# Optimization experiments

Hardware: AMD Instinct MI355X
Metric: run time of the kernel (lower is better)

## Reference

```python
import jax, jax.numpy as jnp
import numpy as np

D_MODEL = 2048
NUM_HEADS = 16
HEAD_DIM = D_MODEL // NUM_HEADS
SCALE = HEAD_DIM ** -0.5
ALPHA = 1.0


def setup_inputs() -> dict:
    key = jax.random.key(0)
    ks = jax.random.split(key, 9)
    B, T = 2, 2048
    s = 0.02
    w = lambda k: jax.random.normal(k, (D_MODEL, D_MODEL), jnp.float32) * s
    b = lambda k: jax.random.normal(k, (D_MODEL,), jnp.float32) * s
    return {
        'x': jax.random.normal(ks[0], (B, T, D_MODEL), jnp.float32),
        'q_w': w(ks[1]), 'q_b': b(ks[2]),
        'k_w': w(ks[3]), 'k_b': b(ks[4]),
        'v_w': w(ks[5]), 'v_b': b(ks[6]),
        'o_w': w(ks[7]), 'o_b': b(ks[8]),
    }


def reference(x, q_w, q_b, k_w, k_b, v_w, v_b, o_w, o_b):
    B, T, D = x.shape
    H, HD = NUM_HEADS, HEAD_DIM

    def proj_split(w, bias):
        y = x @ w.T + bias  # torch Linear: x @ W^T + b
        # B T (H D) -> (B H) T D
        return y.reshape(B, T, H, HD).transpose(0, 2, 1, 3).reshape(B * H, T, HD)

    Q = proj_split(q_w, q_b)
    K = proj_split(k_w, k_b)
    V = proj_split(v_w, v_b)

    # Note: original computes S[h,i,j] = K_i . Q_j (K first, Q second)
    S = jnp.einsum('hid,hjd->hij', K, Q) * SCALE  # (B*H, T, T)

    idx = jnp.arange(T)
    delta = idx[:, None] - idx[None, :]  # delta[i,j] = i - j
    # similarity_power_law decay: -(delta**alpha) for delta>=0, else 0
    decay = jnp.where(delta < 0, 0.0, -(delta.astype(jnp.float32) ** ALPHA))
    # causal mask: positions with j > i (delta < 0) set to -inf, then add decay
    S = jnp.where(delta < 0, -jnp.inf, S) + decay

    C = jax.nn.softmax(S, axis=-1)
    attn = jnp.einsum('hij,hjd->hid', C, V)  # (B*H, T, HD)
    # (B H) T D -> B T (H D)
    attn = attn.reshape(B, H, T, HD).transpose(0, 2, 1, 3).reshape(B, T, D)
    return attn @ o_w.T + o_b
```

## Files before the change

kernel.cpp:

```cpp
#include <hip/hip_runtime.h>
#include <hip/hip_bf16.h>
#include <stdint.h>

#define BT    4096
#define DM    2048
#define TSEQ  2048
#define NHEAD 16
#define HD    128
#define QKV_LD 6144
#define ATT_SCALE 0.088388347648318447f
#define WIN   64

typedef __attribute__((ext_vector_type(8))) short short8;
typedef __attribute__((ext_vector_type(4))) float f32x4;

__device__ __forceinline__ uint16_t f2bf(float f) {
  uint32_t u = __float_as_uint(f);
  return (uint16_t)((u + 0x7FFFu + ((u >> 16) & 1u)) >> 16);
}

__device__ __forceinline__ void gload_lds16(const void* g, void* l) {
  __builtin_amdgcn_global_load_lds((__attribute__((address_space(1))) void*)g,
                                   (__attribute__((address_space(3))) void*)l,
                                   16, 0, 0);
}

__global__ __launch_bounds__(256) void prep(const float* __restrict__ x,
                                            const float* __restrict__ qw,
                                            const float* __restrict__ kw,
                                            const float* __restrict__ vw,
                                            const float* __restrict__ ow,
                                            const float* __restrict__ qb,
                                            const float* __restrict__ kb,
                                            const float* __restrict__ vb,
                                            uint16_t* __restrict__ xb,
                                            uint16_t* __restrict__ wqkv,
                                            uint16_t* __restrict__ wo,
                                            float* __restrict__ bcat) {
  const int NX = BT * DM / 4;
  const int NW = DM * DM / 4;
  const int total = NX + 4 * NW;
  int i0 = blockIdx.x * 256 + threadIdx.x;
  for (int idx = i0; idx < total; idx += gridDim.x * 256) {
    const float* src;
    uint16_t* dst;
    int off;
    if (idx < NX)            { src = x;  dst = xb;                          off = idx; }
    else if (idx < NX + NW)  { src = qw; dst = wqkv;                        off = idx - NX; }
    else if (idx < NX + 2*NW){ src = kw; dst = wqkv + (size_t)DM * DM;      off = idx - NX - NW; }
    else if (idx < NX + 3*NW){ src = vw; dst = wqkv + (size_t)2 * DM * DM;  off = idx - NX - 2*NW; }
    else                     { src = ow; dst = wo;                          off = idx - NX - 3*NW; }
    float4 v = ((const float4*)src)[off];
    ushort4 o;
    o.x = f2bf(v.x); o.y = f2bf(v.y); o.z = f2bf(v.z); o.w = f2bf(v.w);
    ((ushort4*)dst)[off] = o;
  }
  if (i0 < 3 * DM) {
    float v = (i0 < DM) ? qb[i0] : (i0 < 2 * DM ? kb[i0 - DM] : vb[i0 - 2 * DM]);
    bcat[i0] = v;
  }
}

__global__ __launch_bounds__(512, 1) void gemm384(const uint16_t* __restrict__ A,
                                                  const uint16_t* __restrict__ B,
                                                  const float* __restrict__ bias,
                                                  uint16_t* __restrict__ Cout) {
  __shared__ uint16_t sm[81920];

  const int tid = threadIdx.x;
  const int l   = tid & 63;
  const int wid = tid >> 6;
  const int wr  = wid >> 2;
  const int wc  = wid & 3;
  const int ln  = l & 15;
  const int g   = l >> 4;

  const int bid = blockIdx.x;
  const int xcd = bid & 7;
  const int idx = bid >> 3;
  const int m0  = ((xcd >> 2) * 8 + (idx >> 2)) << 8;
  const int n0  = ((xcd & 3) * 4 + (idx & 3)) * 384;

  const int s_r = wid * 8 + (l >> 3);
  const int s_c = ((l & 7) ^ ((wid * 4 + (l >> 4)) & 7)) << 3;
  const uint16_t* gA = A + (size_t)(m0 + s_r) * DM + s_c;
  const uint16_t* gB = B + (size_t)(n0 + s_r) * DM + s_c;
  const int sdst = wid * 512;

  const int key  = (ln >> 1) & 7;
  const int pc0  = (g ^ key) << 3;
  const int pc1  = ((4 + g) ^ key) << 3;
  const int aoff = (wr * 128 + ln) * 64;
  const int boff = 16384 + (wc * 96 + ln) * 64;

  f32x4 acc[8][6];
#pragma unroll
  for (int i = 0; i < 8; ++i)
#pragma unroll
    for (int j = 0; j < 6; ++j) acc[i][j] = (f32x4){0.f, 0.f, 0.f, 0.f};

  const int nt = DM >> 6;

#define STA(T, U)                                                                \
  if ((T) < nt) {                                                                \
    const uint16_t* s_ = gA + (size_t)((U) * 128) * DM + (size_t)(T) * 64;       \
    uint16_t* d_ = sm + ((T) & 1) * 40960 + (U) * 8192 + sdst;                   \
    gload_lds16(s_, d_);                                                         \
    gload_lds16(s_ + (size_t)64 * DM, d_ + 4096);                                \
  }
#define STB(T, U)                                                                \
  if ((T) < nt) {                                                                \
    const uint16_t* s_ = gB + (size_t)((U) * 128) * DM + (size_t)(T) * 64;       \
    uint16_t* d_ = sm + ((T) & 1) * 40960 + 16384 + (U) * 8192 + sdst;           \
    gload_lds16(s_, d_);                                                         \
    gload_lds16(s_ + (size_t)64 * DM, d_ + 4096);                                \
  }
#define FENCE() asm volatile("" ::: "memory")

#define MMH(BUFP, MH, PC)                                                        \
  __builtin_amdgcn_s_setprio(1);                                                 \
  _Pragma("unroll")                                                              \
  for (int mi = 0; mi < 4; ++mi) {                                               \
    short8 af = *(const short8*)((BUFP) + aoff + ((MH) * 64 + mi * 16) * 64 + (PC)); \
    _Pragma("unroll")                                                            \
    for (int nj = 0; nj < 6; ++nj)                                               \
      acc[(MH) * 4 + mi][nj] = __builtin_amdgcn_mfma_f32_16x16x32_bf16(          \
          af, bf[nj], acc[(MH) * 4 + mi][nj], 0, 0, 0);                          \
  }                                                                              \
  __builtin_amdgcn_s_setprio(0);

  STA(0, 0); STA(0, 1);
  STB(0, 0); STB(0, 1); STB(0, 2);
  STB(1, 0); STB(1, 1); STB(1, 2);
  asm volatile("s_waitcnt vmcnt(6)" ::: "memory");
  FENCE(); __builtin_amdgcn_s_barrier(); FENCE();

#pragma unroll 1
  for (int t = 0; t < nt; ++t) {
    const uint16_t* bufp = sm + (size_t)(t & 1) * 40960;
    short8 bf[6];
#pragma unroll
    for (int nj = 0; nj < 6; ++nj)
      bf[nj] = *(const short8*)(bufp + boff + nj * 1024 + pc0);
    STA(t + 1, 0);
    MMH(bufp, 0, pc0);
    STA(t + 1, 1);
    MMH(bufp, 1, pc0);
#pragma unroll
    for (int nj = 0; nj < 6; ++nj)
      bf[nj] = *(const short8*)(bufp + boff + nj * 1024 + pc1);
    MMH(bufp, 0, pc1);
    FENCE(); __builtin_amdgcn_s_barrier(); FENCE();
    STB(t + 2, 0); STB(t + 2, 1); STB(t + 2, 2);
    MMH(bufp, 1, pc1);
    FENCE();
    if (t < nt - 2)       asm volatile("s_waitcnt vmcnt(6)" ::: "memory");
    else if (t == nt - 2) asm volatile("s_waitcnt vmcnt(0)" ::: "memory");
    __builtin_amdgcn_s_barrier(); FENCE();
  }
#undef MMH
#undef STA
#undef STB

  const int g4 = g * 4;
#pragma unroll
  for (int a = 0; a < 8; ++a) {
    size_t row = (size_t)(m0 + wr * 128 + (a >> 2) * 64 + (a & 3) * 16 + g4);
#pragma unroll
    for (int nj = 0; nj < 6; ++nj) {
      int col = n0 + wc * 96 + nj * 16 + ln;
      float bv = bias[col];
#pragma unroll
      for (int r = 0; r < 4; ++r)
        Cout[(row + r) * QKV_LD + col] = f2bf(acc[a][nj][r] + bv);
    }
  }
}

__global__ __launch_bounds__(512, 1) void gemmO(const uint16_t* __restrict__ A,
                                                const uint16_t* __restrict__ B,
                                                const float* __restrict__ bias,
                                                float* __restrict__ Cout) {
  __shared__ uint16_t sm[49152];

  const int tid = threadIdx.x;
  const int l   = tid & 63;
  const int wid = tid >> 6;
  const int wr  = wid >> 2;
  const int wc  = wid & 3;
  const int ln  = l & 15;
  const int g   = l >> 4;

  const int bid = blockIdx.x;
  const int xcd = bid & 7;
  const int idx = bid >> 3;
  const int m0  = ((xcd >> 2) * 8 + (idx >> 2)) << 8;
  const int n0  = ((xcd & 3) * 4 + (idx & 3)) << 7;

  const int s_r = wid * 8 + (l >> 3);
  const int s_c = ((l & 7) ^ ((wid * 4 + (l >> 4)) & 7)) << 3;
  const uint16_t* gA = A + (size_t)(m0 + s_r) * DM + s_c;
  const uint16_t* gB = B + (size_t)(n0 + s_r) * DM + s_c;
  const int sdst = wid * 512;

  const int key  = (ln >> 1) & 7;
  const int pc0  = (g ^ key) << 3;
  const int pc1  = ((4 + g) ^ key) << 3;
  const int aoff = (wr * 128 + ln) * 64;
  const int boff = 16384 + (wc * 32 + ln) * 64;

  f32x4 acc[8][2];
#pragma unroll
  for (int i = 0; i < 8; ++i)
#pragma unroll
    for (int j = 0; j < 2; ++j) acc[i][j] = (f32x4){0.f, 0.f, 0.f, 0.f};

  const int nt = DM >> 6;

#define STA(T, U)                                                                \
  if ((T) < nt) {                                                                \
    const uint16_t* s_ = gA + (size_t)((U) * 128) * DM + (size_t)(T) * 64;       \
    uint16_t* d_ = sm + ((T) & 1) * 24576 + (U) * 8192 + sdst;                   \
    gload_lds16(s_, d_);                                                         \
    gload_lds16(s_ + (size_t)64 * DM, d_ + 4096);                                \
  }
#define STB(T)                                                                   \
  if ((T) < nt) {                                                                \
    const uint16_t* s_ = gB + (size_t)(T) * 64;                                  \
    uint16_t* d_ = sm + ((T) & 1) * 24576 + 16384 + sdst;                        \
    gload_lds16(s_, d_);                                                         \
    gload_lds16(s_ + (size_t)64 * DM, d_ + 4096);                                \
  }
#define FENCE() asm volatile("" ::: "memory")

#define MMH(BUFP, MH, PC)                                                        \
  __builtin_amdgcn_s_setprio(1);                                                 \
  _Pragma("unroll")                                                              \
  for (int mi = 0; mi < 4; ++mi) {                                               \
    short8 af = *(const short8*)((BUFP) + aoff + ((MH) * 64 + mi * 16) * 64 + (PC)); \
    _Pragma("unroll")                                                            \
    for (int nj = 0; nj < 2; ++nj)                                               \
      acc[(MH) * 4 + mi][nj] = __builtin_amdgcn_mfma_f32_16x16x32_bf16(          \
          af, bf[nj], acc[(MH) * 4 + mi][nj], 0, 0, 0);                          \
  }                                                                              \
  __builtin_amdgcn_s_setprio(0);

  STA(0, 0); STA(0, 1);
  STB(0);
  STB(1);
  asm volatile("s_waitcnt vmcnt(2)" ::: "memory");
  FENCE(); __builtin_amdgcn_s_barrier(); FENCE();

#pragma unroll 1
  for (int t = 0; t < nt; ++t) {
    const uint16_t* bufp = sm + (size_t)(t & 1) * 24576;
    short8 bf[2];
#pragma unroll
    for (int nj = 0; nj < 2; ++nj)
      bf[nj] = *(const short8*)(bufp + boff + nj * 1024 + pc0);
    STA(t + 1, 0);
    MMH(bufp, 0, pc0);
    STA(t + 1, 1);
    MMH(bufp, 1, pc0);
#pragma unroll
    for (int nj = 0; nj < 2; ++nj)
      bf[nj] = *(const short8*)(bufp + boff + nj * 1024 + pc1);
    MMH(bufp, 0, pc1);
    FENCE(); __builtin_amdgcn_s_barrier(); FENCE();
    STB(t + 2);
    MMH(bufp, 1, pc1);
    FENCE();
    if (t < nt - 2)       asm volatile("s_waitcnt vmcnt(2)" ::: "memory");
    else if (t == nt - 2) asm volatile("s_waitcnt vmcnt(0)" ::: "memory");
    __builtin_amdgcn_s_barrier(); FENCE();
  }
#undef MMH
#undef STA
#undef STB
#undef FENCE

  const int g4 = g * 4;
#pragma unroll
  for (int a = 0; a < 8; ++a) {
    size_t row = (size_t)(m0 + wr * 128 + (a >> 2) * 64 + (a & 3) * 16 + g4);
#pragma unroll
    for (int nj = 0; nj < 2; ++nj) {
      int col = n0 + wc * 32 + nj * 16 + ln;
      float bv = bias[col];
#pragma unroll
      for (int r = 0; r < 4; ++r)
        Cout[(row + r) * DM + col] = acc[a][nj][r] + bv;
    }
  }
}

__global__ __launch_bounds__(256) void attn_mfma(const uint16_t* __restrict__ QKV,
                                                 uint16_t* __restrict__ O) {
  __shared__ __align__(16) uint16_t smem[16384 + 17408];
  uint16_t* Qs = smem;
  uint16_t* Vt = smem + 16384;
  uint16_t* Pl = smem;

  const int tid  = threadIdx.x;
  const int lane = tid & 63;
  const int w    = tid >> 6;
  const int g    = lane >> 4;
  const int ln   = lane & 15;

  const int i0 = blockIdx.x * 64;
  const int h  = blockIdx.y;
  const int b  = blockIdx.z;
  const int wb = i0 - 63;
  const size_t hoff  = (size_t)h * HD;
  const size_t bbase = (size_t)b * TSEQ;

#pragma unroll
  for (int it = 0; it < 8; ++it) {
    int s   = it * 256 + tid;
    int row = s >> 4, c = s & 15;
    int j = wb + row;
    if (j >= 0 && j < TSEQ) {
      const uint16_t* gsrc = QKV + (bbase + j) * (size_t)QKV_LD + hoff
                           + (size_t)((c ^ (row & 7)) * 8);
      uint16_t* ldst = Qs + (size_t)(s & ~63) * 8;
      gload_lds16(gsrc, ldst);
    } else {
      uint4 z = {0, 0, 0, 0};
      *(uint4*)(Qs + (size_t)s * 8) = z;
    }
  }

#pragma unroll
  for (int it = 0; it < 4; ++it) {
    int s  = it * 256 + tid;
    int jp = (s & 15) | (it << 4);
    int dc = (s >> 4) & 15;
    int j0 = wb + 2 * jp;
    uint4 va = {0, 0, 0, 0}, vb = {0, 0, 0, 0};
    if (j0 >= 0 && j0 < TSEQ)
      va = *(const uint4*)(QKV + (bbase + j0) * (size_t)QKV_LD + 2 * DM + hoff + dc * 8);
    if (j0 + 1 >= 0 && j0 + 1 < TSEQ)
      vb = *(const uint4*)(QKV + (bbase + j0 + 1) * (size_t)QKV_LD + 2 * DM + hoff + dc * 8);
    const uint16_t* ap = (const uint16_t*)&va;
    const uint16_t* bp = (const uint16_t*)&vb;
#pragma unroll
    for (int t = 0; t < 8; ++t) {
      uint32_t pk = (uint32_t)ap[t] | ((uint32_t)bp[t] << 16);
      *(uint32_t*)(Vt + (size_t)(dc * 8 + t) * 136 + 2 * jp) = pk;
    }
  }

  short8 kreg[4];
  {
    const uint16_t* kp = QKV + (bbase + i0 + w * 16 + ln) * (size_t)QKV_LD
                       + DM + hoff + g * 8;
#pragma unroll
    for (int kc = 0; kc < 4; ++kc) kreg[kc] = *(const short8*)(kp + kc * 32);
  }

  __syncthreads();

  f32x4 acc[8];
#pragma unroll
  for (int nf = 0; nf < 8; ++nf) acc[nf] = (f32x4){0.f, 0.f, 0.f, 0.f};
#pragma unroll
  for (int kc = 0; kc < 4; ++kc) {
#pragma unroll
    for (int nf = 0; nf < 8; ++nf) {
      int row = nf * 16 + ln;
      int chunk = (kc * 4 + g) ^ (row & 7);
      short8 qf = *(const short8*)(Qs + (size_t)row * 128 + chunk * 8);
      acc[nf] = __builtin_amdgcn_mfma_f32_16x16x32_bf16(kreg[kc], qf, acc[nf], 0, 0, 0);
    }
  }

#pragma unroll
  for (int nf = 0; nf < 8; ++nf) {
    int rj = nf * 16 + ln;
    int jg = wb + rj;
#pragma unroll
    for (int r = 0; r < 4; ++r) {
      int il = w * 16 + g * 4 + r;
      int delta = il + 63 - rj;
      float v = acc[nf][r] * ATT_SCALE - (float)delta;
      acc[nf][r] = ((unsigned)delta < 64u && jg >= 0) ? v : -1e30f;
    }
  }

  float inv[4];
#pragma unroll
  for (int r = 0; r < 4; ++r) {
    float mx = acc[0][r];
#pragma unroll
    for (int nf = 1; nf < 8; ++nf) mx = fmaxf(mx, acc[nf][r]);
    mx = fmaxf(mx, __shfl_xor(mx, 1));
    mx = fmaxf(mx, __shfl_xor(mx, 2));
    mx = fmaxf(mx, __shfl_xor(mx, 4));
    mx = fmaxf(mx, __shfl_xor(mx, 8));
    float s = 0.f;
#pragma unroll
    for (int nf = 0; nf < 8; ++nf) {
      float e = __expf(acc[nf][r] - mx);
      acc[nf][r] = e;
      s += e;
    }
    s += __shfl_xor(s, 1);
    s += __shfl_xor(s, 2);
    s += __shfl_xor(s, 4);
    s += __shfl_xor(s, 8);
    inv[r] = 1.0f / s;
  }

  __syncthreads();

#pragma unroll
  for (int nf = 0; nf < 8; ++nf)
#pragma unroll
    for (int r = 0; r < 4; ++r)
      Pl[(size_t)(w * 16 + g * 4 + r) * 136 + nf * 16 + ln] = f2bf(acc[nf][r]);
  asm volatile("s_waitcnt lgkmcnt(0)" ::: "memory");
  __builtin_amdgcn_sched_barrier(0);

  f32x4 o[8];
#pragma unroll
  for (int nf = 0; nf < 8; ++nf) o[nf] = (f32x4){0.f, 0.f, 0.f, 0.f};
#pragma unroll
  for (int kc = 0; kc < 4; ++kc) {
    short8 pa = *(const short8*)(Pl + (size_t)(w * 16 + ln) * 136 + kc * 32 + g * 8);
#pragma unroll
    for (int nf = 0; nf < 8; ++nf) {
      short8 vbf = *(const short8*)(Vt + (size_t)(nf * 16 + ln) * 136 + kc * 32 + g * 8);
      o[nf] = __builtin_amdgcn_mfma_f32_16x16x32_bf16(pa, vbf, o[nf], 0, 0, 0);
    }
  }

  const size_t obase = (bbase + i0 + w * 16) * (size_t)DM + hoff;
#pragma unroll
  for (int nf = 0; nf < 8; ++nf)
#pragma unroll
    for (int r = 0; r < 4; ++r)
      O[obase + (size_t)(g * 4 + r) * DM + nf * 16 + ln] = f2bf(o[nf][r] * inv[r]);
}

extern "C" void kernel_launch(void* const* d_in, const int* in_sizes, int n_in,
                              void* d_out, int out_size, void* d_ws, size_t ws_size,
                              hipStream_t stream) {
  const float* x   = (const float*)d_in[0];
  const float* q_w = (const float*)d_in[1];
  const float* q_b = (const float*)d_in[2];
  const float* k_w = (const float*)d_in[3];
  const float* k_b = (const float*)d_in[4];
  const float* v_w = (const float*)d_in[5];
  const float* v_b = (const float*)d_in[6];
  const float* o_w = (const float*)d_in[7];
  const float* o_b = (const float*)d_in[8];

  char* ws = (char*)d_ws;
  const size_t XB_BYTES   = (size_t)BT * DM * 2;
  const size_t W_BYTES    = (size_t)DM * DM * 2;
  const size_t WQKV_BYTES = 3 * W_BYTES;

  uint16_t* xb   = (uint16_t*)(ws);
  uint16_t* wqkv = (uint16_t*)(ws + XB_BYTES);
  uint16_t* wo   = (uint16_t*)(ws + XB_BYTES + WQKV_BYTES);
  float*    bcat = (float*)   (ws + XB_BYTES + WQKV_BYTES + W_BYTES);
  uint16_t* QKVb = (uint16_t*)(ws + XB_BYTES + WQKV_BYTES + W_BYTES + 24576);

  prep<<<2048, 256, 0, stream>>>(x, q_w, k_w, v_w, o_w, q_b, k_b, v_b,
                                 xb, wqkv, wo, bcat);

  gemm384<<<256, 512, 0, stream>>>(xb, wqkv, bcat, QKVb);

  dim3 ga(TSEQ / 64, NHEAD, 2);
  attn_mfma<<<ga, 256, 0, stream>>>(QKVb, xb);

  gemmO<<<256, 512, 0, stream>>>(xb, wo, o_b, (float*)d_out);
}
```

Measured before the change: 172.3 us.

## Load A operand of output GEMM directly into registers, stage only B in LDS

The output projection GEMM now reads its A fragments straight from global memory into registers, prefetching the next k-tile into a second register set, instead of staging A through LDS. LDS is used only for B, shrinking shared memory from 96KB to 32KB and removing A's LDS reads. The aim is to cut LDS traffic and bandwidth pressure in the main loop. In exchange it raises register pressure (32 short8 fragments held live) and relies on direct, less coalesced global loads. Each A row is also read redundantly by the four column waves that share it.

```diff
diff --git a/kernel.cpp b/kernel.cpp
--- a/kernel.cpp
+++ b/kernel.cpp
@@ -177,11 +177,11 @@
   }
 }
 
-__global__ __launch_bounds__(512, 1) void gemmO(const uint16_t* __restrict__ A,
-                                                const uint16_t* __restrict__ B,
-                                                const float* __restrict__ bias,
-                                                float* __restrict__ Cout) {
-  __shared__ uint16_t sm[49152];
+__global__ __launch_bounds__(512, 1) void gemmO3(const uint16_t* __restrict__ A,
+                                                 const uint16_t* __restrict__ B,
+                                                 const float* __restrict__ bias,
+                                                 float* __restrict__ Cout) {
+  __shared__ uint16_t sm[16384];
 
   const int tid = threadIdx.x;
   const int l   = tid & 63;
@@ -197,17 +197,17 @@
   const int m0  = ((xcd >> 2) * 8 + (idx >> 2)) << 8;
   const int n0  = ((xcd & 3) * 4 + (idx & 3)) << 7;
 
+  const uint16_t* gAf = A + (size_t)(m0 + wr * 128 + ln) * DM + (g << 3);
+
   const int s_r = wid * 8 + (l >> 3);
   const int s_c = ((l & 7) ^ ((wid * 4 + (l >> 4)) & 7)) << 3;
-  const uint16_t* gA = A + (size_t)(m0 + s_r) * DM + s_c;
   const uint16_t* gB = B + (size_t)(n0 + s_r) * DM + s_c;
   const int sdst = wid * 512;
 
   const int key  = (ln >> 1) & 7;
   const int pc0  = (g ^ key) << 3;
   const int pc1  = ((4 + g) ^ key) << 3;
-  const int aoff = (wr * 128 + ln) * 64;
-  const int boff = 16384 + (wc * 32 + ln) * 64;
+  const int boff = (wc * 32 + ln) * 64;
 
   f32x4 acc[8][2];
 #pragma unroll
@@ -217,79 +217,88 @@
 
   const int nt = DM >> 6;
 
-#define STA(T, U)                                                                \
+#define STB3(T)                                                                  \
   if ((T) < nt) {                                                                \
-    const uint16_t* s_ = gA + (size_t)((U) * 128) * DM + (size_t)(T) * 64;       \
-    uint16_t* d_ = sm + ((T) & 1) * 24576 + (U) * 8192 + sdst;                   \
+    const uint16_t* s_ = gB + (size_t)(T) * 64;                                  \
+    uint16_t* d_ = sm + ((T) & 1) * 8192 + sdst;                                 \
     gload_lds16(s_, d_);                                                         \
     gload_lds16(s_ + (size_t)64 * DM, d_ + 4096);                                \
   }
-#define STB(T)                                                                   \
-  if ((T) < nt) {                                                                \
-    const uint16_t* s_ = gB + (size_t)(T) * 64;                                  \
-    uint16_t* d_ = sm + ((T) & 1) * 24576 + 16384 + sdst;                        \
-    gload_lds16(s_, d_);                                                         \
-    gload_lds16(s_ + (size_t)64 * DM, d_ + 4096);                                \
-  }
 #define FENCE() asm volatile("" ::: "memory")
 
-#define MMH(BUFP, MH, PC)                                                        \
-  __builtin_amdgcn_s_setprio(1);                                                 \
-  _Pragma("unroll")                                                              \
-  for (int mi = 0; mi < 4; ++mi) {                                               \
-    short8 af = *(const short8*)((BUFP) + aoff + ((MH) * 64 + mi * 16) * 64 + (PC)); \
-    _Pragma("unroll")                                                            \
-    for (int nj = 0; nj < 2; ++nj)                                               \
-      acc[(MH) * 4 + mi][nj] = __builtin_amdgcn_mfma_f32_16x16x32_bf16(          \
-          af, bf[nj], acc[(MH) * 4 + mi][nj], 0, 0, 0);                          \
-  }                                                                              \
-  __builtin_amdgcn_s_setprio(0);
-
-  STA(0, 0); STA(0, 1);
-  STB(0);
-  STB(1);
+  short8 a_[8][2], an_[8][2];
+#pragma unroll
+  for (int mi = 0; mi < 8; ++mi)
+#pragma unroll
+    for (int kk = 0; kk < 2; ++kk)
+      a_[mi][kk] = *(const short8*)(gAf + (size_t)mi * 16 * DM + kk * 32);
+  STB3(0);
+  STB3(1);
   asm volatile("s_waitcnt vmcnt(2)" ::: "memory");
   FENCE(); __builtin_amdgcn_s_barrier(); FENCE();
 
 #pragma unroll 1
   for (int t = 0; t < nt; ++t) {
-    const uint16_t* bufp = sm + (size_t)(t & 1) * 24576;
+    const uint16_t* bufp = sm + (size_t)(t & 1) * 8192;
+    if (t + 1 < nt) {
+#pragma unroll
+      for (int mi = 0; mi < 8; ++mi)
+#pragma unroll
+        for (int kk = 0; kk < 2; ++kk)
+          an_[mi][kk] = *(const short8*)(gAf + (size_t)mi * 16 * DM
+                                         + (size_t)(t + 1) * 64 + kk * 32);
+    }
     short8 bf[2];
 #pragma unroll
     for (int nj = 0; nj < 2; ++nj)
       bf[nj] = *(const short8*)(bufp + boff + nj * 1024 + pc0);
-    STA(t + 1, 0);
-    MMH(bufp, 0, pc0);
-    STA(t + 1, 1);
-    MMH(bufp, 1, pc0);
+    __builtin_amdgcn_s_setprio(1);
+#pragma unroll
+    for (int mi = 0; mi < 8; ++mi)
+#pragma unroll
+      for (int nj = 0; nj < 2; ++nj)
+        acc[mi][nj] = __builtin_amdgcn_mfma_f32_16x16x32_bf16(
+            a_[mi][0], bf[nj], acc[mi][nj], 0, 0, 0);
+    __builtin_amdgcn_s_setprio(0);
 #pragma unroll
     for (int nj = 0; nj < 2; ++nj)
       bf[nj] = *(const short8*)(bufp + boff + nj * 1024 + pc1);
-    MMH(bufp, 0, pc1);
+    __builtin_amdgcn_s_setprio(1);
+#pragma unroll
+    for (int mi = 0; mi < 8; ++mi)
+#pragma unroll
+      for (int nj = 0; nj < 2; ++nj)
+        acc[mi][nj] = __builtin_amdgcn_mfma_f32_16x16x32_bf16(
+            a_[mi][1], bf[nj], acc[mi][nj], 0, 0, 0);
+    __builtin_amdgcn_s_setprio(0);
     FENCE(); __builtin_amdgcn_s_barrier(); FENCE();
-    STB(t + 2);
-    MMH(bufp, 1, pc1);
+    STB3(t + 2);
     FENCE();
     if (t < nt - 2)       asm volatile("s_waitcnt vmcnt(2)" ::: "memory");
     else if (t == nt - 2) asm volatile("s_waitcnt vmcnt(0)" ::: "memory");
     __builtin_amdgcn_s_barrier(); FENCE();
-  }
-#undef MMH
-#undef STA
-#undef STB
+    if (t + 1 < nt) {
+#pragma unroll
+      for (int mi = 0; mi < 8; ++mi)
+#pragma unroll
+        for (int kk = 0; kk < 2; ++kk)
+          a_[mi][kk] = an_[mi][kk];
+    }
+  }
+#undef STB3
 #undef FENCE
 
   const int g4 = g * 4;
 #pragma unroll
-  for (int a = 0; a < 8; ++a) {
-    size_t row = (size_t)(m0 + wr * 128 + (a >> 2) * 64 + (a & 3) * 16 + g4);
+  for (int mi = 0; mi < 8; ++mi) {
+    size_t row = (size_t)(m0 + wr * 128 + mi * 16 + g4);
 #pragma unroll
     for (int nj = 0; nj < 2; ++nj) {
       int col = n0 + wc * 32 + nj * 16 + ln;
       float bv = bias[col];
 #pragma unroll
       for (int r = 0; r < 4; ++r)
-        Cout[(row + r) * DM + col] = acc[a][nj][r] + bv;
+        Cout[(row + r) * DM + col] = acc[mi][nj][r] + bv;
     }
   }
 }
@@ -474,5 +483,5 @@
   dim3 ga(TSEQ / 64, NHEAD, 2);
   attn_mfma<<<ga, 256, 0, stream>>>(QKVb, xb);
 
-  gemmO<<<256, 512, 0, stream>>>(xb, wo, o_b, (float*)d_out);
-}
+  gemmO3<<<256, 512, 0, stream>>>(xb, wo, o_b, (float*)d_out);
+}
```

Result: slower. 275.3 us, median of 2 (+59.7%).
